# Kernel tuning notes

Measured on AMD Instinct MI355X. Metric: run time of the kernel, lower is better.

## Reference

```python
import jax, jax.numpy as jnp
import numpy as np

NUM_HEADS = 8

def setup_inputs() -> dict:
    key = jax.random.key(0)
    ks = jax.random.split(key, 12)
    B, C, H, W = 4, 256, 64, 64
    QK = 256
    NSP = 256
    x = jax.random.normal(ks[0], (B, C, H, W), dtype=jnp.float32)
    affinity_matrix = jax.random.uniform(ks[1], (B, NSP, H * W), dtype=jnp.float32)
    norm_w = 1.0 + 0.02 * jax.random.normal(ks[2], (C,), dtype=jnp.float32)
    norm_b = 0.02 * jax.random.normal(ks[3], (C,), dtype=jnp.float32)
    Wq = 0.02 * jax.random.normal(ks[4], (QK, C), dtype=jnp.float32)
    Wk = 0.02 * jax.random.normal(ks[5], (QK, C), dtype=jnp.float32)
    Wv = 0.02 * jax.random.normal(ks[6], (C, C), dtype=jnp.float32)
    Wsp = 0.02 * jax.random.normal(ks[7], (QK, C), dtype=jnp.float32)
    lepe_w = 0.02 * jax.random.normal(ks[8], (C, 1, 3, 3), dtype=jnp.float32)  # depthwise OIHW
    lepe_b = 0.02 * jax.random.normal(ks[9], (C,), dtype=jnp.float32)
    return {"x": x, "affinity_matrix": affinity_matrix, "norm_w": norm_w,
            "norm_b": norm_b, "Wq": Wq, "Wk": Wk, "Wv": Wv, "Wsp": Wsp,
            "lepe_w": lepe_w, "lepe_b": lepe_b, "num_spixels": NSP}


def _layernorm2d(x, w, b, eps=1e-6):
    # LayerNorm over channel dim of NCHW input
    xp = x.transpose(0, 2, 3, 1)  # B,H,W,C
    mu = xp.mean(-1, keepdims=True)
    var = ((xp - mu) ** 2).mean(-1, keepdims=True)
    xn = (xp - mu) * jax.lax.rsqrt(var + eps) * w + b
    return xn.transpose(0, 3, 1, 2)


def _sgca(x, affinity_matrix, norm_w, norm_b, Wq, Wk, Wv, Wsp, lepe_w, lepe_b, num_spixels):
    B, C, H, W = x.shape
    HW = H * W
    h = NUM_HEADS
    qk_dim = Wq.shape[0]
    dqk = qk_dim // h
    dv = C // h
    scale = (C // h) ** -0.5

    xn = _layernorm2d(x, norm_w, norm_b)

    # superpixel aggregation: b (hw) c
    x_flat = xn.reshape(B, C, HW).transpose(0, 2, 1)  # B,HW,C
    stoken = jnp.einsum('bmn,bnc->bmc', affinity_matrix, x_flat)
    stoken = stoken / (affinity_matrix.sum(-1, keepdims=True) + 1e-16)  # B,nsp,C

    # sp projection -> B,h,dqk,nsp
    st = jnp.einsum('bmc,qc->bmq', stoken, Wsp).transpose(0, 2, 1)
    st = st.reshape(B, h, dqk, num_spixels)

    # 1x1 conv projections
    q = jnp.einsum('oc,bchw->bohw', Wq, xn).reshape(B, h, dqk, HW)
    k = jnp.einsum('oc,bchw->bohw', Wk, xn).reshape(B, h, dqk, HW)
    vx = jnp.einsum('oc,bchw->bohw', Wv, xn)  # B,C,H,W
    v = vx.reshape(B, h, dv, HW)

    # LePE: depthwise 3x3 conv on v(x)
    lepe = jax.lax.conv_general_dilated(
        vx, lepe_w, window_strides=(1, 1), padding=((1, 1), (1, 1)),
        feature_group_count=C, dimension_numbers=('NCHW', 'OIHW', 'NCHW'))
    lepe = lepe + lepe_b[None, :, None, None]
    # faithful to original: [B,C,HW] -> permute -> [B,HW,C] -> reshape B,C,H,W
    lepe = lepe.reshape(B, C, HW).transpose(0, 2, 1).reshape(B, C, H, W)

    # stage 1: k^T @ stoken, softmax over HW axis
    s_attn = jnp.einsum('bhdn,bhdm->bhnm', k, st) * scale  # B,h,HW,nsp
    s_attn = jax.nn.softmax(s_attn, axis=-2)
    s_out = jnp.einsum('bhdn,bhnm->bhdm', v, s_attn)  # B,h,dv,nsp

    # stage 2: stoken^T @ q, softmax over nsp axis
    x_attn = jnp.einsum('bhdm,bhdn->bhmn', st, q) * scale  # B,h,nsp,HW
    x_attn = jax.nn.softmax(x_attn, axis=-2)
    x_out = jnp.einsum('bhdm,bhmn->bhdn', s_out, x_attn).reshape(B, C, H, W)

    return x_out + lepe


def reference(x, affinity_matrix, norm_w, norm_b, Wq, Wk, Wv, Wsp, lepe_w, lepe_b, num_spixels):
    return _sgca(x, affinity_matrix, norm_w, norm_b, Wq, Wk, Wv, Wsp, lepe_w, lepe_b, num_spixels)
```

## Files before the change

kernel.cpp:

```cpp
#include <hip/hip_runtime.h>
#include <hip/hip_bf16.h>

#define BATCH 4
#define CCH   256
#define HWHW  4096
#define NSP   256
#define NHEAD 8
#define SCALE 0.17677669529663689f
#define PLANE 1048576L

typedef short bf16x8 __attribute__((ext_vector_type(8)));
typedef float f32x4  __attribute__((ext_vector_type(4)));

__global__ __launch_bounds__(256)
void ln_fused_kernel(const float* __restrict__ x, const float* __restrict__ w,
                     const float* __restrict__ bb,
                     const float* __restrict__ Wq, const float* __restrict__ Wk,
                     const float* __restrict__ Wv, const float* __restrict__ Wsp,
                     const float* __restrict__ aff,
                     __hip_bfloat16* __restrict__ xn_cn,
                     __hip_bfloat16* __restrict__ xn_nc,
                     __hip_bfloat16* __restrict__ wbf,
                     __hip_bfloat16* __restrict__ aff_bf)
{
    __shared__ __hip_bfloat16 xs[256][72];
    __shared__ float ps[4][64], pss[4][64], mus[64], rstds[64];
    __shared__ float wls[256], bls[256];
    int blk = blockIdx.x;
    int t = threadIdx.x;
    if (blk >= 256) {
        int sel = blk - 256;
        if (sel < 4) {
            const float* src = (sel == 0) ? Wq : (sel == 1) ? Wk : (sel == 2) ? Wv : Wsp;
            __hip_bfloat16* dst = wbf + sel * 65536;
            for (int i = t * 4; i < 65536; i += 1024) {
                float4 f = *(const float4*)(src + i);
                __hip_bfloat16 p[4];
                p[0] = __float2bfloat16(f.x); p[1] = __float2bfloat16(f.y);
                p[2] = __float2bfloat16(f.z); p[3] = __float2bfloat16(f.w);
                *(int2*)(dst + i) = *(int2*)p;
            }
        } else {
            long base = (long)(sel - 4) * 65536;
            for (int i = t * 4; i < 65536; i += 1024) {
                float4 f = *(const float4*)(aff + base + i);
                __hip_bfloat16 p[4];
                p[0] = __float2bfloat16(f.x); p[1] = __float2bfloat16(f.y);
                p[2] = __float2bfloat16(f.z); p[3] = __float2bfloat16(f.w);
                *(int2*)(aff_bf + base + i) = *(int2*)p;
            }
        }
        return;
    }
    int b = blk >> 6;
    int n0 = (blk & 63) * 64;
    int p = t & 63, cq = t >> 6;
    wls[t] = w[t]; bls[t] = bb[t];
    long base = (long)b * CCH * HWHW + n0 + p;
    float s = 0.f, ss = 0.f;
#pragma unroll 8
    for (int i = 0; i < 64; ++i) {
        int c = cq * 64 + i;
        float v = x[base + (long)c * HWHW];
        xs[c][p] = __float2bfloat16(v);
        s += v; ss += v * v;
    }
    ps[cq][p] = s; pss[cq][p] = ss;
    __syncthreads();
    if (cq == 0) {
        float S  = ps[0][p] + ps[1][p] + ps[2][p] + ps[3][p];
        float SS = pss[0][p] + pss[1][p] + pss[2][p] + pss[3][p];
        float mu = S * (1.f / 256.f);
        float var = SS * (1.f / 256.f) - mu * mu;
        mus[p] = mu; rstds[p] = rsqrtf(var + 1e-6f);
    }
    __syncthreads();
    float mu = mus[p], rstd = rstds[p];
#pragma unroll
    for (int c8 = 0; c8 < 8; ++c8) {
        short pack[8];
#pragma unroll
        for (int j = 0; j < 8; ++j) {
            int c = cq * 64 + c8 * 8 + j;
            float v = ((float)xs[c][p] - mu) * rstd * wls[c] + bls[c];
            __hip_bfloat16 bv = __float2bfloat16(v);
            xs[c][p] = bv;
            pack[j] = *(short*)&bv;
        }
        *(int4*)(xn_nc + ((long)b * HWHW + n0 + p) * CCH + cq * 64 + c8 * 8) = *(int4*)pack;
    }
    __syncthreads();
#pragma unroll
    for (int i = 0; i < 8; ++i) {
        int idx = t + i * 256;
        int c = idx >> 3, seg = idx & 7;
        *(int4*)(xn_cn + (long)(b * CCH + c) * HWHW + n0 + seg * 8) =
            *(const int4*)&xs[c][seg * 8];
    }
}

__global__ __launch_bounds__(256)
void reduce8_cast_kernel(const float* __restrict__ part, const float* __restrict__ rsPart,
                         __hip_bfloat16* __restrict__ out, float* __restrict__ rs)
{
    int i = blockIdx.x * 256 + threadIdx.x;
    if (blockIdx.x < 4) {
        int b = i >> 8, m = i & 255;
        float s = 0.f;
#pragma unroll
        for (int ch = 0; ch < 8; ++ch) s += rsPart[((b * 8 + ch) << 8) + m];
        rs[i] = s;
    }
    int b = i >> 16, idx = i & 65535;
    long base = (long)b * 8 * 65536 + idx;
    float s = 0.f;
#pragma unroll
    for (int ch = 0; ch < 8; ++ch) s += part[base + (long)ch * 65536];
    out[i] = __float2bfloat16(s);
}

template <int OUTK, bool ROWSCALE, bool ROWSUM>
__global__ __launch_bounds__(256)
void mfma_gemm_nt(const __hip_bfloat16* __restrict__ A, const __hip_bfloat16* __restrict__ B,
                  void* __restrict__ Cptr, int N, int K, int kChunk, int kShift,
                  long aStrideZ, long bStrideZ, long cStrideZ,
                  const float* __restrict__ rowScale, long sStrideZ,
                  float* __restrict__ rsPart)
{
    __shared__ __hip_bfloat16 Asm[4 * 64 * 8];
    __shared__ __hip_bfloat16 Bsm[4 * 64 * 8];
    int z = blockIdx.z;
    int b = z >> kShift;
    int ch = z & ((1 << kShift) - 1);
    int t = threadIdx.x;
    int lane = t & 63, w = t >> 6;
    int l15 = lane & 15, quad = lane >> 4;
    int Mt = blockIdx.y * 64, Nt = blockIdx.x * 64;

    const __hip_bfloat16* aSrc = A + b * aStrideZ + (long)ch * kChunk
        + (long)(Mt + w * 16 + l15) * K + quad * 8;
    const __hip_bfloat16* bSrc = B + b * bStrideZ + (long)ch * kChunk
        + (long)(Nt + w * 16 + l15) * K + quad * 8;
    __hip_bfloat16* aDst = &Asm[t * 8];
    __hip_bfloat16* bDst = &Bsm[t * 8];

    f32x4 acc00 = {0.f,0.f,0.f,0.f}, acc01 = acc00, acc10 = acc00, acc11 = acc00;
    f32x4 rs0 = acc00, rs1 = acc00;
    bf16x8 onesf;
    { short o = (l15 == 0) ? (short)0x3F80 : (short)0;
      onesf = bf16x8{o, o, o, o, o, o, o, o}; }
    int wm = (w & 1) * 2, wn = (w >> 1) * 2;

    int4 aReg = *(const int4*)aSrc;
    int4 bReg = *(const int4*)bSrc;
    for (int k0 = 0; k0 < kChunk; k0 += 32) {
        *(int4*)aDst = aReg;
        *(int4*)bDst = bReg;
        __syncthreads();
        if (k0 + 32 < kChunk) {
            aSrc += 32; bSrc += 32;
            aReg = *(const int4*)aSrc;
            bReg = *(const int4*)bSrc;
        }
        bf16x8 a0 = ((const bf16x8*)Asm)[wm * 64 + lane];
        bf16x8 a1 = ((const bf16x8*)Asm)[(wm + 1) * 64 + lane];
        bf16x8 b0 = ((const bf16x8*)Bsm)[wn * 64 + lane];
        bf16x8 b1 = ((const bf16x8*)Bsm)[(wn + 1) * 64 + lane];
        acc00 = __builtin_amdgcn_mfma_f32_16x16x32_bf16(a0, b0, acc00, 0, 0, 0);
        acc01 = __builtin_amdgcn_mfma_f32_16x16x32_bf16(a0, b1, acc01, 0, 0, 0);
        acc10 = __builtin_amdgcn_mfma_f32_16x16x32_bf16(a1, b0, acc10, 0, 0, 0);
        acc11 = __builtin_amdgcn_mfma_f32_16x16x32_bf16(a1, b1, acc11, 0, 0, 0);
        if (ROWSUM) {
            rs0 = __builtin_amdgcn_mfma_f32_16x16x32_bf16(a0, onesf, rs0, 0, 0, 0);
            rs1 = __builtin_amdgcn_mfma_f32_16x16x32_bf16(a1, onesf, rs1, 0, 0, 0);
        }
        __syncthreads();
    }
    if (ROWSUM && blockIdx.x == 0 && (w >> 1) == 0 && l15 == 0) {
#pragma unroll
        for (int r = 0; r < 4; ++r) {
            rsPart[(long)z * 256 + Mt + wm * 16 + quad * 4 + r]       = rs0[r];
            rsPart[(long)z * 256 + Mt + (wm + 1) * 16 + quad * 4 + r] = rs1[r];
        }
    }
    f32x4 accs[2][2] = {{acc00, acc01}, {acc10, acc11}};
#pragma unroll
    for (int i = 0; i < 2; ++i)
#pragma unroll
        for (int j = 0; j < 2; ++j)
#pragma unroll
            for (int r = 0; r < 4; ++r) {
                int m = Mt + (wm + i) * 16 + quad * 4 + r;
                int n = Nt + (wn + j) * 16 + l15;
                float val = accs[i][j][r];
                if (ROWSCALE) val /= (rowScale[(long)b * sStrideZ + m] + 1e-16f);
                long off = (long)z * cStrideZ + (long)m * N + n;
                if (OUTK == 0) ((float*)Cptr)[off] = val;
                else ((__hip_bfloat16*)Cptr)[off] = __float2bfloat16(val);
            }
}

__global__ __launch_bounds__(256)
void stage1_mfma(const __hip_bfloat16* __restrict__ qk_nc,
                 const __hip_bfloat16* __restrict__ v_cn,
                 const __hip_bfloat16* __restrict__ st_md,
                 __hip_bfloat16* __restrict__ opart)
{
    __shared__ __hip_bfloat16 Es[256 * 72];
    __shared__ __hip_bfloat16 sts[256 * 40];
    const int chunk = blockIdx.x, bh = blockIdx.y;
    const int b = bh >> 3, h = bh & 7;
    const int t = threadIdx.x, lane = t & 63, w = t >> 6;
    const int l15 = lane & 15, quad = lane >> 4;
    const int n0 = chunk * 256;

    {
        const int4* src = (const int4*)(st_md + ((long)(b * 256 + t)) * 256 + h * 32);
        int4* dst = (int4*)&sts[t * 40];
        dst[0] = src[0]; dst[1] = src[1]; dst[2] = src[2]; dst[3] = src[3];
    }
    __syncthreads();
    bf16x8 afrag[16];
#pragma unroll
    for (int mt = 0; mt < 16; ++mt)
        afrag[mt] = *(const bf16x8*)&sts[(mt * 16 + l15) * 40 + quad * 8];
    bf16x8 onesf;
    { short o = (l15 == 0) ? (short)0x3F80 : (short)0;
      onesf = bf16x8{o, o, o, o, o, o, o, o}; }

    f32x4 occ[4][3];
#pragma unroll
    for (int i = 0; i < 4; ++i)
#pragma unroll
        for (int j = 0; j < 3; ++j) occ[i][j] = f32x4{0.f,0.f,0.f,0.f};

    for (int sub = 0; sub < 4; ++sub) {
        const int nbase = n0 + sub * 64;
        bf16x8 kf = *(const bf16x8*)(qk_nc + ((long)b * 4096 + nbase + 16 * w + l15) * 512 + 256 + h * 32 + quad * 8);
#pragma unroll
        for (int mt = 0; mt < 16; ++mt) {
            f32x4 s = __builtin_amdgcn_mfma_f32_16x16x32_bf16(afrag[mt], kf, f32x4{0.f,0.f,0.f,0.f}, 0, 0, 0);
#pragma unroll
            for (int r = 0; r < 4; ++r)
                Es[(mt * 16 + quad * 4 + r) * 72 + 16 * w + l15] =
                    __float2bfloat16(__expf(s[r] * SCALE));
        }
        __syncthreads();
#pragma unroll
        for (int ks = 0; ks < 2; ++ks) {
            bf16x8 bf0 = *(const bf16x8*)(v_cn + ((long)(b * 256 + h * 32 + l15)) * 4096 + nbase + ks * 32 + quad * 8);
            bf16x8 bf1 = *(const bf16x8*)(v_cn + ((long)(b * 256 + h * 32 + 16 + l15)) * 4096 + nbase + ks * 32 + quad * 8);
#pragma unroll
            for (int mi = 0; mi < 4; ++mi) {
                bf16x8 af = *(const bf16x8*)&Es[(64 * w + mi * 16 + l15) * 72 + ks * 32 + quad * 8];
                occ[mi][0] = __builtin_amdgcn_mfma_f32_16x16x32_bf16(af, bf0, occ[mi][0], 0, 0, 0);
                occ[mi][1] = __builtin_amdgcn_mfma_f32_16x16x32_bf16(af, bf1, occ[mi][1], 0, 0, 0);
                occ[mi][2] = __builtin_amdgcn_mfma_f32_16x16x32_bf16(af, onesf, occ[mi][2], 0, 0, 0);
            }
        }
        __syncthreads();
    }
    __hip_bfloat16* tb = Es;
#pragma unroll
    for (int mi = 0; mi < 4; ++mi)
#pragma unroll
        for (int jt = 0; jt < 3; ++jt) {
            if (jt == 2 && l15 != 0) continue;
            int col = jt * 16 + l15;
#pragma unroll
            for (int r = 0; r < 4; ++r) {
                int m = 64 * w + mi * 16 + quad * 4 + r;
                tb[col * 264 + m] = __float2bfloat16(occ[mi][jt][r]);
            }
        }
    __syncthreads();
    int* og = (int*)(opart) + (long)(chunk * 32 + bh) * 4224;
    const int* tbi = (const int*)tb;
#pragma unroll
    for (int i = 0; i < 17; ++i) {
        int idx = t + i * 256;
        if (idx < 4224) {
            int row = idx >> 7, off = idx & 127;
            og[idx] = tbi[row * 132 + off];
        }
    }
}

__global__ __launch_bounds__(256)
void merge1_kernel(const __hip_bfloat16* __restrict__ opart, __hip_bfloat16* __restrict__ sout)
{
    int t = blockIdx.x * 256 + threadIdx.x;
    int m = t & 255;
    int d = (t >> 8) & 31;
    int bh = t >> 13;
    float num = 0.f, den = 0.f;
    for (int ch = 0; ch < 16; ++ch) {
        long base = (long)((ch * 32 + bh) * 33) * 256 + m;
        num += (float)opart[base + (long)d * 256];
        den += (float)opart[base + 32 * 256];
    }
    sout[(long)bh * 8192 + d * 256 + m] = __float2bfloat16(num / den);
}

__global__ __launch_bounds__(256)
void lepe_conv_t_kernel(const __hip_bfloat16* __restrict__ v_cn,
                        const float* __restrict__ lw, const float* __restrict__ lb,
                        __hip_bfloat16* __restrict__ lepe_cn)
{
    __shared__ __hip_bfloat16 in_t[32 * 384];
    __shared__ __hip_bfloat16 tile_bf[256 * 33];
    __shared__ float wls[288], bls[32];
    const int bx = blockIdx.x;
    const int c0 = blockIdx.y * 32;
    const int b  = blockIdx.z;
    const int t = threadIdx.x;
    const int n0 = bx * 256, r0 = bx * 4;

    for (int i = t; i < 288; i += 256) wls[i] = lw[c0 * 9 + i];
    if (t < 32)  bls[t] = lb[c0 + t];
#pragma unroll
    for (int i = 0; i < 6; ++i) {
        int vi = t + i * 256;
        int ch = vi / 48;
        int off = (vi % 48) * 8;
        int g = (r0 - 1) * 64 + off;
        int4 val = {0, 0, 0, 0};
        if ((unsigned)g < 4096u)
            val = *(const int4*)(v_cn + (((long)(b * CCH + c0 + ch)) << 12) + g);
        *(int4*)&in_t[ch * 384 + off] = val;
    }
    __syncthreads();

    const int lane = t & 63, w = t >> 6;
#pragma unroll
    for (int i = 0; i < 8; ++i) {
        int ch = w * 8 + i;
        float cr[6], lf[6], rf[6];
#pragma unroll
        for (int rr = 0; rr < 6; ++rr) {
            cr[rr] = (float)in_t[ch * 384 + rr * 64 + lane];
            float lv = __shfl_up(cr[rr], 1);
            float rv = __shfl_down(cr[rr], 1);
            lf[rr] = (lane == 0) ? 0.f : lv;
            rf[rr] = (lane == 63) ? 0.f : rv;
        }
        float w0 = wls[ch*9+0], w1 = wls[ch*9+1], w2 = wls[ch*9+2];
        float w3 = wls[ch*9+3], w4 = wls[ch*9+4], w5 = wls[ch*9+5];
        float w6 = wls[ch*9+6], w7 = wls[ch*9+7], w8 = wls[ch*9+8];
        float bias = bls[ch];
#pragma unroll
        for (int r = 0; r < 4; ++r) {
            float acc = bias
                + lf[r]   * w0 + cr[r]   * w1 + rf[r]   * w2
                + lf[r+1] * w3 + cr[r+1] * w4 + rf[r+1] * w5
                + lf[r+2] * w6 + cr[r+2] * w7 + rf[r+2] * w8;
            tile_bf[(r * 64 + lane) * 33 + ch] = __float2bfloat16(acc);
        }
    }
    __syncthreads();
#pragma unroll
    for (int i = 0; i < 32; ++i) {
        int idx = t + i * 256;
        int nl = idx >> 5, cj = idx & 31;
        int sp = n0 + nl;
        lepe_cn[((long)(b * CCH + (sp >> 4)) << 12) + (nl & 15) * 256 + c0 + cj] =
            tile_bf[nl * 33 + cj];
    }
}

__global__ __launch_bounds__(256)
void stage2_mfma(const __hip_bfloat16* __restrict__ qk_nc,
                 const __hip_bfloat16* __restrict__ st_md,
                 const __hip_bfloat16* __restrict__ sout_bf,
                 const __hip_bfloat16* __restrict__ lepe_cn,
                 float* __restrict__ out)
{
    __shared__ __hip_bfloat16 Es2[64 * 264];
    __shared__ __hip_bfloat16 sts[256 * 40];
    __shared__ __hip_bfloat16 sos[32 * 264];
    __shared__ float o_t[32 * 68];
    const int chunk = blockIdx.x, bh = blockIdx.y;
    const int b = bh >> 3, h = bh & 7;
    const int t = threadIdx.x, lane = t & 63, w = t >> 6;
    const int l15 = lane & 15, quad = lane >> 4;
    const int n0 = chunk * 256;

    {
        const int4* src = (const int4*)(st_md + ((long)(b * 256 + t)) * 256 + h * 32);
        int4* dst = (int4*)&sts[t * 40];
        dst[0] = src[0]; dst[1] = src[1]; dst[2] = src[2]; dst[3] = src[3];
    }
    {
        int row = t >> 3, seg = t & 7;
        const int4* src = (const int4*)(sout_bf + (long)bh * 8192 + row * 256 + seg * 32);
        int4* dst = (int4*)&sos[row * 264 + seg * 32];
        dst[0] = src[0]; dst[1] = src[1]; dst[2] = src[2]; dst[3] = src[3];
    }
    __syncthreads();
    bf16x8 stfrag[4];
#pragma unroll
    for (int mt = 0; mt < 4; ++mt)
        stfrag[mt] = *(const bf16x8*)&sts[(64 * w + mt * 16 + l15) * 40 + quad * 8];
    bf16x8 onesf;
    { short o = (l15 == 0) ? (short)0x3F80 : (short)0;
      onesf = bf16x8{o, o, o, o, o, o, o, o}; }

    for (int sub = 0; sub < 4; ++sub) {
        const int nbase = n0 + sub * 64;
#pragma unroll
        for (int nt = 0; nt < 4; ++nt) {
            bf16x8 qf = *(const bf16x8*)(qk_nc + ((long)b * 4096 + nbase + nt * 16 + l15) * 512 + h * 32 + quad * 8);
#pragma unroll
            for (int mt = 0; mt < 4; ++mt) {
                f32x4 s = __builtin_amdgcn_mfma_f32_16x16x32_bf16(qf, stfrag[mt], f32x4{0.f,0.f,0.f,0.f}, 0, 0, 0);
#pragma unroll
                for (int r = 0; r < 4; ++r)
                    Es2[(nt * 16 + quad * 4 + r) * 264 + 64 * w + mt * 16 + l15] =
                        __float2bfloat16(__expf(s[r] * SCALE));
            }
        }
        __syncthreads();
        f32x4 o0 = {0.f,0.f,0.f,0.f}, o1 = o0, o2 = o0;
#pragma unroll
        for (int ks = 0; ks < 8; ++ks) {
            bf16x8 af = *(const bf16x8*)&Es2[(16 * w + l15) * 264 + ks * 32 + quad * 8];
            bf16x8 b0 = *(const bf16x8*)&sos[(l15) * 264 + ks * 32 + quad * 8];
            bf16x8 b1 = *(const bf16x8*)&sos[(16 + l15) * 264 + ks * 32 + quad * 8];
            o0 = __builtin_amdgcn_mfma_f32_16x16x32_bf16(af, b0, o0, 0, 0, 0);
            o1 = __builtin_amdgcn_mfma_f32_16x16x32_bf16(af, b1, o1, 0, 0, 0);
            o2 = __builtin_amdgcn_mfma_f32_16x16x32_bf16(af, onesf, o2, 0, 0, 0);
        }
        __syncthreads();
#pragma unroll
        for (int r = 0; r < 4; ++r) {
            float den = __shfl(o2[r], lane & 48);
            float inv = 1.f / den;
            o_t[(l15) * 68 + 16 * w + quad * 4 + r]      = o0[r] * inv;
            o_t[(16 + l15) * 68 + 16 * w + quad * 4 + r] = o1[r] * inv;
        }
        __syncthreads();
        {
            int row = t >> 3, coff = (t & 7) * 8;
            long gb = ((long)(b * 256 + h * 32 + row)) * 4096 + nbase + coff;
            int4 lp4 = *(const int4*)(lepe_cn + gb);
            const __hip_bfloat16* lp = (const __hip_bfloat16*)&lp4;
            const float* sp = &o_t[row * 68 + coff];
            float4 r0, r1;
            r0.x = sp[0] + (float)lp[0]; r0.y = sp[1] + (float)lp[1];
            r0.z = sp[2] + (float)lp[2]; r0.w = sp[3] + (float)lp[3];
            r1.x = sp[4] + (float)lp[4]; r1.y = sp[5] + (float)lp[5];
            r1.z = sp[6] + (float)lp[6]; r1.w = sp[7] + (float)lp[7];
            *(float4*)(out + gb)     = r0;
            *(float4*)(out + gb + 4) = r1;
        }
        __syncthreads();
    }
}

extern "C" void kernel_launch(void* const* d_in, const int* in_sizes, int n_in,
                              void* d_out, int out_size, void* d_ws, size_t ws_size,
                              hipStream_t stream)
{
    const float* x    = (const float*)d_in[0];
    const float* aff  = (const float*)d_in[1];
    const float* nw   = (const float*)d_in[2];
    const float* nb   = (const float*)d_in[3];
    const float* Wq   = (const float*)d_in[4];
    const float* Wk   = (const float*)d_in[5];
    const float* Wv   = (const float*)d_in[6];
    const float* Wsp  = (const float*)d_in[7];
    const float* lw   = (const float*)d_in[8];
    const float* lb   = (const float*)d_in[9];
    float* out = (float*)d_out;

    float* ws = (float*)d_ws;
    const long P = PLANE;
    __hip_bfloat16* qk_nc  = (__hip_bfloat16*)(ws);
    __hip_bfloat16* v_cn   = (__hip_bfloat16*)(ws + 4 * P);
    __hip_bfloat16* xn_cn  = (__hip_bfloat16*)(ws + 6 * P);
    __hip_bfloat16* xn_nc  = (__hip_bfloat16*)(ws + 8 * P);
    __hip_bfloat16* lepe_cn= (__hip_bfloat16*)(ws + 10 * P);
    __hip_bfloat16* aff_bf = (__hip_bfloat16*)(ws + 12 * P);
    float* stoken_part = ws + 14 * P;
    __hip_bfloat16* opart = (__hip_bfloat16*)(ws + 16 * P);
    float* tail        = ws + 16 * P + 2162688;
    __hip_bfloat16* wbf       = (__hip_bfloat16*)tail;
    __hip_bfloat16* stoken_bf = (__hip_bfloat16*)(tail + 131072);
    __hip_bfloat16* st_md     = (__hip_bfloat16*)(tail + 262144);
    __hip_bfloat16* sout_bf   = (__hip_bfloat16*)(tail + 393216);
    float* rs      = tail + 524288;
    float* rs_part = tail + 525312;

    ln_fused_kernel<<<324, 256, 0, stream>>>(x, nw, nb, Wq, Wk, Wv, Wsp, aff,
                                             xn_cn, xn_nc, wbf, aff_bf);
    mfma_gemm_nt<0, false, true><<<dim3(4, 4, 32), 256, 0, stream>>>(
        aff_bf, xn_cn, stoken_part, 256, 4096, 512, 3, P, P, 65536L, nullptr, 0, rs_part);
    reduce8_cast_kernel<<<1024, 256, 0, stream>>>(stoken_part, rs_part, stoken_bf, rs);
    mfma_gemm_nt<1, true, false><<<dim3(4, 4, 4), 256, 0, stream>>>(
        stoken_bf, wbf + 3 * 65536, st_md, 256, 256, 256, 0, 65536L, 0L, 65536L, rs, 256L, nullptr);
    mfma_gemm_nt<1, false, false><<<dim3(8, 64, 4), 256, 0, stream>>>(
        xn_nc, wbf, qk_nc, 512, 256, 256, 0, P, 0L, 2 * P, nullptr, 0, nullptr);
    mfma_gemm_nt<1, false, false><<<dim3(64, 4, 4), 256, 0, stream>>>(
        wbf + 2 * 65536, xn_nc, v_cn, 4096, 256, 256, 0, 0L, P, P, nullptr, 0, nullptr);
    lepe_conv_t_kernel<<<dim3(16, 8, BATCH), 256, 0, stream>>>(v_cn, lw, lb, lepe_cn);
    stage1_mfma<<<dim3(16, 32), 256, 0, stream>>>(qk_nc, v_cn, st_md, opart);
    merge1_kernel<<<1024, 256, 0, stream>>>(opart, sout_bf);
    stage2_mfma<<<dim3(16, 32), 256, 0, stream>>>(qk_nc, st_md, sout_bf, lepe_cn, out);
}
```

Baseline: 213.1 us.

## Fuse affinity bf16 conversion into stoken GEMM and restructure LayerNorm kernel

The affinity matrix is no longer pre-cast to bf16 in the LayerNorm kernel. The stoken GEMM now reads fp32 affinity directly and converts it while staging into shared memory. This removes an extra write and read of a 4M-element bf16 buffer, at the cost of doubling the A-operand global read bytes inside the GEMM. The LayerNorm kernel is also rewritten to use 512 threads with float4 register loads, and it drops the shared-memory transpose tile in favour of direct vectorized stores to both layouts.

```diff
diff --git a/kernel.cpp b/kernel.cpp
--- a/kernel.cpp
+++ b/kernel.cpp
@@ -10,93 +10,95 @@
 #define PLANE 1048576L
 
 typedef short bf16x8 __attribute__((ext_vector_type(8)));
+typedef short bf16x4 __attribute__((ext_vector_type(4)));
 typedef float f32x4  __attribute__((ext_vector_type(4)));
 
-__global__ __launch_bounds__(256)
+__device__ __forceinline__ short f2bs(float f) {
+    __hip_bfloat16 h = __float2bfloat16(f);
+    return *(short*)&h;
+}
+__device__ __forceinline__ bf16x8 cvt8(float4 a, float4 b) {
+    bf16x8 p;
+    p[0] = f2bs(a.x); p[1] = f2bs(a.y); p[2] = f2bs(a.z); p[3] = f2bs(a.w);
+    p[4] = f2bs(b.x); p[5] = f2bs(b.y); p[6] = f2bs(b.z); p[7] = f2bs(b.w);
+    return p;
+}
+
+__global__ __launch_bounds__(512)
 void ln_fused_kernel(const float* __restrict__ x, const float* __restrict__ w,
                      const float* __restrict__ bb,
                      const float* __restrict__ Wq, const float* __restrict__ Wk,
                      const float* __restrict__ Wv, const float* __restrict__ Wsp,
-                     const float* __restrict__ aff,
                      __hip_bfloat16* __restrict__ xn_cn,
                      __hip_bfloat16* __restrict__ xn_nc,
-                     __hip_bfloat16* __restrict__ wbf,
-                     __hip_bfloat16* __restrict__ aff_bf)
-{
-    __shared__ __hip_bfloat16 xs[256][72];
-    __shared__ float ps[4][64], pss[4][64], mus[64], rstds[64];
+                     __hip_bfloat16* __restrict__ wbf)
+{
+    __shared__ float ps[32][64], pss[32][64];
+    __shared__ float mus[64], rstds[64];
     __shared__ float wls[256], bls[256];
     int blk = blockIdx.x;
     int t = threadIdx.x;
     if (blk >= 256) {
         int sel = blk - 256;
-        if (sel < 4) {
-            const float* src = (sel == 0) ? Wq : (sel == 1) ? Wk : (sel == 2) ? Wv : Wsp;
-            __hip_bfloat16* dst = wbf + sel * 65536;
-            for (int i = t * 4; i < 65536; i += 1024) {
-                float4 f = *(const float4*)(src + i);
-                __hip_bfloat16 p[4];
-                p[0] = __float2bfloat16(f.x); p[1] = __float2bfloat16(f.y);
-                p[2] = __float2bfloat16(f.z); p[3] = __float2bfloat16(f.w);
-                *(int2*)(dst + i) = *(int2*)p;
-            }
-        } else {
-            long base = (long)(sel - 4) * 65536;
-            for (int i = t * 4; i < 65536; i += 1024) {
-                float4 f = *(const float4*)(aff + base + i);
-                __hip_bfloat16 p[4];
-                p[0] = __float2bfloat16(f.x); p[1] = __float2bfloat16(f.y);
-                p[2] = __float2bfloat16(f.z); p[3] = __float2bfloat16(f.w);
-                *(int2*)(aff_bf + base + i) = *(int2*)p;
-            }
+        const float* src = (sel == 0) ? Wq : (sel == 1) ? Wk : (sel == 2) ? Wv : Wsp;
+        __hip_bfloat16* dst = wbf + sel * 65536;
+        for (int i = t * 4; i < 65536; i += 2048) {
+            float4 f = *(const float4*)(src + i);
+            __hip_bfloat16 p[4];
+            p[0] = __float2bfloat16(f.x); p[1] = __float2bfloat16(f.y);
+            p[2] = __float2bfloat16(f.z); p[3] = __float2bfloat16(f.w);
+            *(int2*)(dst + i) = *(int2*)p;
         }
         return;
     }
     int b = blk >> 6;
     int n0 = (blk & 63) * 64;
-    int p = t & 63, cq = t >> 6;
-    wls[t] = w[t]; bls[t] = bb[t];
-    long base = (long)b * CCH * HWHW + n0 + p;
-    float s = 0.f, ss = 0.f;
-#pragma unroll 8
-    for (int i = 0; i < 64; ++i) {
-        int c = cq * 64 + i;
-        float v = x[base + (long)c * HWHW];
-        xs[c][p] = __float2bfloat16(v);
-        s += v; ss += v * v;
-    }
-    ps[cq][p] = s; pss[cq][p] = ss;
-    __syncthreads();
-    if (cq == 0) {
-        float S  = ps[0][p] + ps[1][p] + ps[2][p] + ps[3][p];
-        float SS = pss[0][p] + pss[1][p] + pss[2][p] + pss[3][p];
+    int pg = t & 15;
+    int cq = t >> 4;
+    if (t < 256) { wls[t] = w[t]; bls[t] = bb[t]; }
+
+    const float* xp = x + ((long)(b * CCH + cq * 8)) * HWHW + n0 + pg * 4;
+    float4 v[8];
+#pragma unroll
+    for (int i = 0; i < 8; ++i) v[i] = *(const float4*)(xp + (long)i * HWHW);
+    float4 s = {0.f,0.f,0.f,0.f}, ss = {0.f,0.f,0.f,0.f};
+#pragma unroll
+    for (int i = 0; i < 8; ++i) {
+        s.x += v[i].x; s.y += v[i].y; s.z += v[i].z; s.w += v[i].w;
+        ss.x += v[i].x * v[i].x; ss.y += v[i].y * v[i].y;
+        ss.z += v[i].z * v[i].z; ss.w += v[i].w * v[i].w;
+    }
+    *(float4*)&ps[cq][pg * 4]  = s;
+    *(float4*)&pss[cq][pg * 4] = ss;
+    __syncthreads();
+    if (t < 64) {
+        float S = 0.f, SS = 0.f;
+#pragma unroll
+        for (int q = 0; q < 32; ++q) { S += ps[q][t]; SS += pss[q][t]; }
         float mu = S * (1.f / 256.f);
         float var = SS * (1.f / 256.f) - mu * mu;
-        mus[p] = mu; rstds[p] = rsqrtf(var + 1e-6f);
-    }
-    __syncthreads();
-    float mu = mus[p], rstd = rstds[p];
-#pragma unroll
-    for (int c8 = 0; c8 < 8; ++c8) {
-        short pack[8];
-#pragma unroll
-        for (int j = 0; j < 8; ++j) {
-            int c = cq * 64 + c8 * 8 + j;
-            float v = ((float)xs[c][p] - mu) * rstd * wls[c] + bls[c];
-            __hip_bfloat16 bv = __float2bfloat16(v);
-            xs[c][p] = bv;
-            pack[j] = *(short*)&bv;
-        }
-        *(int4*)(xn_nc + ((long)b * HWHW + n0 + p) * CCH + cq * 64 + c8 * 8) = *(int4*)pack;
-    }
-    __syncthreads();
+        mus[t] = mu; rstds[t] = rsqrtf(var + 1e-6f);
+    }
+    __syncthreads();
+    float4 mu4 = *(float4*)&mus[pg * 4];
+    float4 rs4 = *(float4*)&rstds[pg * 4];
+
+    bf16x8 pk[4];
 #pragma unroll
     for (int i = 0; i < 8; ++i) {
-        int idx = t + i * 256;
-        int c = idx >> 3, seg = idx & 7;
-        *(int4*)(xn_cn + (long)(b * CCH + c) * HWHW + n0 + seg * 8) =
-            *(const int4*)&xs[c][seg * 8];
-    }
+        int c = cq * 8 + i;
+        float wc = wls[c], bc = bls[c];
+        short h0 = f2bs((v[i].x - mu4.x) * rs4.x * wc + bc);
+        short h1 = f2bs((v[i].y - mu4.y) * rs4.y * wc + bc);
+        short h2 = f2bs((v[i].z - mu4.z) * rs4.z * wc + bc);
+        short h3 = f2bs((v[i].w - mu4.w) * rs4.w * wc + bc);
+        pk[0][i] = h0; pk[1][i] = h1; pk[2][i] = h2; pk[3][i] = h3;
+        bf16x4 q; q[0] = h0; q[1] = h1; q[2] = h2; q[3] = h3;
+        *(bf16x4*)(xn_cn + ((long)(b * CCH + c)) * HWHW + n0 + pg * 4) = q;
+    }
+#pragma unroll
+    for (int j = 0; j < 4; ++j)
+        *(bf16x8*)(xn_nc + ((long)b * HWHW + n0 + pg * 4 + j) * CCH + cq * 8) = pk[j];
 }
 
 __global__ __launch_bounds__(256)
@@ -119,9 +121,9 @@
     out[i] = __float2bfloat16(s);
 }
 
-template <int OUTK, bool ROWSCALE, bool ROWSUM>
+template <int OUTK, bool ROWSCALE, bool ROWSUM, bool AF32>
 __global__ __launch_bounds__(256)
-void mfma_gemm_nt(const __hip_bfloat16* __restrict__ A, const __hip_bfloat16* __restrict__ B,
+void mfma_gemm_nt(const void* __restrict__ Av, const __hip_bfloat16* __restrict__ B,
                   void* __restrict__ Cptr, int N, int K, int kChunk, int kShift,
                   long aStrideZ, long bStrideZ, long cStrideZ,
                   const float* __restrict__ rowScale, long sStrideZ,
@@ -137,8 +139,9 @@
     int l15 = lane & 15, quad = lane >> 4;
     int Mt = blockIdx.y * 64, Nt = blockIdx.x * 64;
 
-    const __hip_bfloat16* aSrc = A + b * aStrideZ + (long)ch * kChunk
-        + (long)(Mt + w * 16 + l15) * K + quad * 8;
+    long aOff = b * aStrideZ + (long)ch * kChunk + (long)(Mt + w * 16 + l15) * K + quad * 8;
+    const __hip_bfloat16* aSrcH = (const __hip_bfloat16*)Av + aOff;
+    const float*          aSrcF = (const float*)Av + aOff;
     const __hip_bfloat16* bSrc = B + b * bStrideZ + (long)ch * kChunk
         + (long)(Nt + w * 16 + l15) * K + quad * 8;
     __hip_bfloat16* aDst = &Asm[t * 8];
@@ -151,16 +154,20 @@
       onesf = bf16x8{o, o, o, o, o, o, o, o}; }
     int wm = (w & 1) * 2, wn = (w >> 1) * 2;
 
-    int4 aReg = *(const int4*)aSrc;
+    int4 aReg; float4 fA0, fA1;
+    if (AF32) { fA0 = *(const float4*)aSrcF; fA1 = *(const float4*)(aSrcF + 4); }
+    else       aReg = *(const int4*)aSrcH;
     int4 bReg = *(const int4*)bSrc;
     for (int k0 = 0; k0 < kChunk; k0 += 32) {
-        *(int4*)aDst = aReg;
+        if (AF32) *(bf16x8*)aDst = cvt8(fA0, fA1);
+        else      *(int4*)aDst = aReg;
         *(int4*)bDst = bReg;
         __syncthreads();
         if (k0 + 32 < kChunk) {
-            aSrc += 32; bSrc += 32;
-            aReg = *(const int4*)aSrc;
+            bSrc += 32;
             bReg = *(const int4*)bSrc;
+            if (AF32) { aSrcF += 32; fA0 = *(const float4*)aSrcF; fA1 = *(const float4*)(aSrcF + 4); }
+            else      { aSrcH += 32; aReg = *(const int4*)aSrcH; }
         }
         bf16x8 a0 = ((const bf16x8*)Asm)[wm * 64 + lane];
         bf16x8 a1 = ((const bf16x8*)Asm)[(wm + 1) * 64 + lane];
@@ -480,7 +487,6 @@
     __hip_bfloat16* xn_cn  = (__hip_bfloat16*)(ws + 6 * P);
     __hip_bfloat16* xn_nc  = (__hip_bfloat16*)(ws + 8 * P);
     __hip_bfloat16* lepe_cn= (__hip_bfloat16*)(ws + 10 * P);
-    __hip_bfloat16* aff_bf = (__hip_bfloat16*)(ws + 12 * P);
     float* stoken_part = ws + 14 * P;
     __hip_bfloat16* opart = (__hip_bfloat16*)(ws + 16 * P);
     float* tail        = ws + 16 * P + 2162688;
@@ -491,16 +497,16 @@
     float* rs      = tail + 524288;
     float* rs_part = tail + 525312;
 
-    ln_fused_kernel<<<324, 256, 0, stream>>>(x, nw, nb, Wq, Wk, Wv, Wsp, aff,
-                                             xn_cn, xn_nc, wbf, aff_bf);
-    mfma_gemm_nt<0, false, true><<<dim3(4, 4, 32), 256, 0, stream>>>(
-        aff_bf, xn_cn, stoken_part, 256, 4096, 512, 3, P, P, 65536L, nullptr, 0, rs_part);
+    ln_fused_kernel<<<260, 512, 0, stream>>>(x, nw, nb, Wq, Wk, Wv, Wsp,
+                                             xn_cn, xn_nc, wbf);
+    mfma_gemm_nt<0, false, true, true><<<dim3(4, 4, 32), 256, 0, stream>>>(
+        aff, xn_cn, stoken_part, 256, 4096, 512, 3, P, P, 65536L, nullptr, 0, rs_part);
     reduce8_cast_kernel<<<1024, 256, 0, stream>>>(stoken_part, rs_part, stoken_bf, rs);
-    mfma_gemm_nt<1, true, false><<<dim3(4, 4, 4), 256, 0, stream>>>(
+    mfma_gemm_nt<1, true, false, false><<<dim3(4, 4, 4), 256, 0, stream>>>(
         stoken_bf, wbf + 3 * 65536, st_md, 256, 256, 256, 0, 65536L, 0L, 65536L, rs, 256L, nullptr);
-    mfma_gemm_nt<1, false, false><<<dim3(8, 64, 4), 256, 0, stream>>>(
+    mfma_gemm_nt<1, false, false, false><<<dim3(8, 64, 4), 256, 0, stream>>>(
         xn_nc, wbf, qk_nc, 512, 256, 256, 0, P, 0L, 2 * P, nullptr, 0, nullptr);
-    mfma_gemm_nt<1, false, false><<<dim3(64, 4, 4), 256, 0, stream>>>(
+    mfma_gemm_nt<1, false, false, false><<<dim3(64, 4, 4), 256, 0, stream>>>(
         wbf + 2 * 65536, xn_nc, v_cn, 4096, 256, 256, 0, 0L, P, P, nullptr, 0, nullptr);
     lepe_conv_t_kernel<<<dim3(16, 8, BATCH), 256, 0, stream>>>(v_cn, lw, lb, lepe_cn);
     stage1_mfma<<<dim3(16, 32), 256, 0, stream>>>(qk_nc, v_cn, st_md, opart);
```

Result: no change. 209.0 us (-1.9%).
